# Kernel optimization log

Hardware: AMD Instinct MI355X
Metric: run time of the kernel (lower is better)

## Reference

```python
import jax, jax.numpy as jnp
import numpy as np

M_B, M_S, D_IN, D_OUT = 4, 2048, 4096, 4096
SPARSITY_KEEP = 0.1


def setup_inputs() -> dict:
    key = jax.random.key(0)
    k1, k2, k3, k4 = jax.random.split(key, 4)
    data = jax.random.normal(k1, (M_B, M_S, D_IN), dtype=jnp.float32)
    weight = jax.random.normal(k2, (D_OUT, D_IN), dtype=jnp.float32) * 0.02
    w_mask = (jax.random.uniform(k3, (D_OUT, D_IN)) < SPARSITY_KEEP).astype(jnp.float32)
    bias_p = jax.random.normal(k4, (D_OUT,), dtype=jnp.float32) * 0.02
    return {"data": data, "weight": weight, "w_mask": w_mask, "bias_p": bias_p}


def reference(data, weight, w_mask, bias_p):
    # Equivalent math to CSR-conversion + sparse GEMM: out = data @ (W*mask)^T + b
    w = weight * w_mask                      # [D_OUT, D_IN]
    out = jnp.einsum('bsk,nk->bsn', data, w)  # [B, S, D_OUT]
    return out + bias_p
```

## Files before the change

### kernel.cpp

```cpp
#include <hip/hip_runtime.h>
#include <hip/hip_bf16.h>


#define M_TOT 8192
#define N_TOT 4096
#define K_TOT 4096

#define BM 256
#define BN 256
#define BK 64
#define NT (K_TOT / BK)

typedef __attribute__((ext_vector_type(8))) short short8;
typedef __attribute__((ext_vector_type(4))) float floatx4;

__device__ inline unsigned short f2bf(float f) {
    unsigned int u = __builtin_bit_cast(unsigned int, f);
    u += 0x7fffu + ((u >> 16) & 1u);
    return (unsigned short)(u >> 16);
}

__global__ __launch_bounds__(256) void cast_data_kernel(const float4* __restrict__ in,
                                                        ushort4* __restrict__ out) {
    int i = blockIdx.x * 256 + threadIdx.x;
    float4 f = in[i];
    ushort4 o;
    o.x = f2bf(f.x); o.y = f2bf(f.y); o.z = f2bf(f.z); o.w = f2bf(f.w);
    out[i] = o;
}

__global__ __launch_bounds__(256) void cast_w_kernel(const float4* __restrict__ w,
                                                     const float4* __restrict__ m,
                                                     ushort4* __restrict__ out) {
    int i = blockIdx.x * 256 + threadIdx.x;
    float4 a = w[i];
    float4 b = m[i];
    ushort4 o;
    o.x = f2bf(a.x * b.x); o.y = f2bf(a.y * b.y);
    o.z = f2bf(a.z * b.z); o.w = f2bf(a.w * b.w);
    out[i] = o;
}

__device__ inline void load_lds16(const unsigned short* g, unsigned short* l) {
    __builtin_amdgcn_global_load_lds(
        (__attribute__((address_space(1))) void*)(const_cast<unsigned short*>(g)),
        (__attribute__((address_space(3))) void*)(l),
        16, 0, 0);
}

#define BAR()   __builtin_amdgcn_s_barrier()
#define SB0()   __builtin_amdgcn_sched_barrier(0)
#define VM8()   asm volatile("s_waitcnt vmcnt(8)" ::: "memory")
#define VM0()   asm volatile("s_waitcnt vmcnt(0)" ::: "memory")

__global__ __launch_bounds__(512, 2) void gemm_bt_kernel(const unsigned short* __restrict__ A,
                                                         const unsigned short* __restrict__ W,
                                                         const float* __restrict__ bias,
                                                         float* __restrict__ out) {
    __shared__ __align__(16) unsigned short As[2 * BM * BK];
    __shared__ __align__(16) unsigned short Bs[2 * BN * BK];

    const int t = threadIdx.x;
    const int m0 = blockIdx.y * BM;
    const int n0 = blockIdx.x * BN;

    const int lane  = t & 63;
    const int wv    = t >> 6;
    const int wm    = (wv >> 2) * 128;
    const int wn    = (wv & 3) * 64;
    const int row16 = lane & 15;
    const int quad  = lane >> 4;
    const int rx    = row16 & 7;

    const int srow  = t >> 3;
    const int lslot = (t & 7) ^ (srow & 7);
    const size_t thr_off = (size_t)srow * K_TOT + (size_t)lslot * 8;

    const unsigned short* Ag = A + (size_t)m0 * K_TOT + thr_off;
    const unsigned short* Bg = W + (size_t)n0 * K_TOT + thr_off;

    auto stageA = [&](int ts, int h) {
        const unsigned short* s = Ag + (size_t)(h * 128) * K_TOT + ts * BK;
        unsigned short* d = As + (ts & 1) * (BM * BK) + h * (128 * BK) + t * 8;
        load_lds16(s, d);
        load_lds16(s + (size_t)64 * K_TOT, d + 512 * 8);
    };
    auto stageB = [&](int ts, int h) {
        const unsigned short* s = Bg + (size_t)(h * 128) * K_TOT + ts * BK;
        unsigned short* d = Bs + (ts & 1) * (BN * BK) + h * (128 * BK) + t * 8;
        load_lds16(s, d);
        load_lds16(s + (size_t)64 * K_TOT, d + 512 * 8);
    };

    short8 aX[4][2], aY[4][2];
    short8 b0[2][2], b1[2][2];

    auto readA = [&](int buf, int mh, short8 (&d)[4][2]) {
#pragma unroll
        for (int i = 0; i < 4; i++) {
            const unsigned short* base =
                As + buf * (BM * BK) + (wm + mh * 64 + i * 16 + row16) * BK;
            d[i][0] = *(const short8*)(base + ((quad ^ rx) << 3));
            d[i][1] = *(const short8*)(base + (((4 + quad) ^ rx) << 3));
        }
    };
    auto readB = [&](int buf, int nh, short8 (&d)[2][2]) {
#pragma unroll
        for (int j = 0; j < 2; j++) {
            const unsigned short* base =
                Bs + buf * (BN * BK) + (wn + nh * 32 + j * 16 + row16) * BK;
            d[j][0] = *(const short8*)(base + ((quad ^ rx) << 3));
            d[j][1] = *(const short8*)(base + (((4 + quad) ^ rx) << 3));
        }
    };

    floatx4 acc[8][4];
#pragma unroll
    for (int i = 0; i < 8; i++)
#pragma unroll
        for (int j = 0; j < 4; j++) {
            floatx4 z = {0.0f, 0.0f, 0.0f, 0.0f};
            acc[i][j] = z;
        }

    auto mmaQ = [&](short8 (&a)[4][2], short8 (&b)[2][2], int mh, int nh) {
        __builtin_amdgcn_s_setprio(1);
#pragma unroll
        for (int i = 0; i < 4; i++)
#pragma unroll
            for (int j = 0; j < 2; j++)
#pragma unroll
                for (int ks = 0; ks < 2; ks++)
                    acc[mh * 4 + i][nh * 2 + j] = __builtin_amdgcn_mfma_f32_16x16x32_bf16(
                        a[i][ks], b[j][ks], acc[mh * 4 + i][nh * 2 + j], 0, 0, 0);
        __builtin_amdgcn_s_setprio(0);
    };

    auto tileT = [&](int kt, short8 (&aC)[4][2], short8 (&aN)[4][2], int mode) {
        const int buf = kt & 1;
        readA(buf, 1, aN);
        mmaQ(aC, b0, 0, 0);
        if (mode != 2) BAR();
        readB(buf, 1, b1);
        if (mode == 0) { stageA(kt + 2, 0); stageB(kt + 2, 0); }
        mmaQ(aN, b0, 1, 0);
        if (mode != 2) BAR();
        if (mode == 0) stageA(kt + 2, 1);
        mmaQ(aN, b1, 1, 1);
        if (mode != 2) BAR();
        if (mode == 0) { stageB(kt + 2, 1); VM8(); }
        else if (mode == 1) { VM0(); }
        if (mode != 2) {
            BAR(); SB0();
            readA(buf ^ 1, 0, aN);
            readB(buf ^ 1, 0, b0);
        }
        mmaQ(aC, b1, 0, 1);
        if (mode != 2) BAR();
    };

    stageA(0, 0); stageB(0, 0); stageA(0, 1); stageB(0, 1);
    stageA(1, 0); stageB(1, 0); stageA(1, 1); stageB(1, 1);
    VM8();
    BAR(); SB0();
    readA(0, 0, aX);
    readB(0, 0, b0);

    for (int kt = 0; kt < NT - 2; kt += 2) {
        tileT(kt,     aX, aY, 0);
        tileT(kt + 1, aY, aX, 0);
    }
    tileT(NT - 2, aX, aY, 1);
    tileT(NT - 1, aY, aX, 2);

    float bb[4];
#pragma unroll
    for (int j = 0; j < 4; j++)
        bb[j] = bias[n0 + wn + j * 16 + row16];

#pragma unroll
    for (int ai = 0; ai < 8; ai++) {
        const int gm = m0 + wm + ai * 16 + quad * 4;
#pragma unroll
        for (int bj = 0; bj < 4; bj++) {
            const int gn = n0 + wn + bj * 16 + row16;
            float* o = out + (size_t)gm * N_TOT + gn;
#pragma unroll
            for (int r = 0; r < 4; r++)
                o[(size_t)r * N_TOT] = acc[ai][bj][r] + bb[bj];
        }
    }
}

extern "C" void kernel_launch(void* const* d_in, const int* in_sizes, int n_in,
                              void* d_out, int out_size, void* d_ws, size_t ws_size,
                              hipStream_t stream) {
    const float* data   = (const float*)d_in[0];
    const float* weight = (const float*)d_in[1];
    const float* w_mask = (const float*)d_in[2];
    const float* bias_p = (const float*)d_in[3];
    float* out = (float*)d_out;

    unsigned short* a_bf = (unsigned short*)d_ws;
    unsigned short* w_bf = a_bf + (size_t)M_TOT * K_TOT;

    cast_data_kernel<<<(M_TOT * K_TOT) / (256 * 4), 256, 0, stream>>>(
        (const float4*)data, (ushort4*)a_bf);
    cast_w_kernel<<<(N_TOT * K_TOT) / (256 * 4), 256, 0, stream>>>(
        (const float4*)weight, (const float4*)w_mask, (ushort4*)w_bf);

    dim3 grid(N_TOT / BN, M_TOT / BM);
    gemm_bt_kernel<<<grid, 512, 0, stream>>>(a_bf, w_bf, bias_p, out);
}
```

Before: 529.9 us.

## Switch GEMM to 32x32x16 MFMA tiles and rework prefetch/barrier schedule

Replaces the 16x16x32 bf16 MFMA fragments with 32x32x16 MFMAs, which changes the LDS read pattern, the register fragment layout and the output write mapping. It also reorders the global-to-LDS staging so that A and B are each issued as a group, uses a vmcnt(4) wait, and removes one barrier per tile. The larger MFMA shape is meant to cut LDS read traffic and instruction count per FLOP. The removed barrier and the reordered waits change the synchronization between LDS buffer reuse and the prefetch, which risks races or stalls.

```diff
diff --git a/kernel.cpp b/kernel.cpp
--- a/kernel.cpp
+++ b/kernel.cpp
@@ -12,7 +12,7 @@
 #define NT (K_TOT / BK)
 
 typedef __attribute__((ext_vector_type(8))) short short8;
-typedef __attribute__((ext_vector_type(4))) float floatx4;
+typedef __attribute__((ext_vector_type(16))) float floatx16;
 
 __device__ inline unsigned short f2bf(float f) {
     unsigned int u = __builtin_bit_cast(unsigned int, f);
@@ -51,6 +51,7 @@
 #define BAR()   __builtin_amdgcn_s_barrier()
 #define SB0()   __builtin_amdgcn_sched_barrier(0)
 #define VM8()   asm volatile("s_waitcnt vmcnt(8)" ::: "memory")
+#define VM4()   asm volatile("s_waitcnt vmcnt(4)" ::: "memory")
 #define VM0()   asm volatile("s_waitcnt vmcnt(0)" ::: "memory")
 
 __global__ __launch_bounds__(512, 2) void gemm_bt_kernel(const unsigned short* __restrict__ A,
@@ -68,9 +69,9 @@
     const int wv    = t >> 6;
     const int wm    = (wv >> 2) * 128;
     const int wn    = (wv & 3) * 64;
-    const int row16 = lane & 15;
-    const int quad  = lane >> 4;
-    const int rx    = row16 & 7;
+    const int l31   = lane & 31;
+    const int khalf = lane >> 5;
+    const int rx    = lane & 7;
 
     const int srow  = t >> 3;
     const int lslot = (t & 7) ^ (srow & 7);
@@ -92,66 +93,62 @@
         load_lds16(s + (size_t)64 * K_TOT, d + 512 * 8);
     };
 
-    short8 aX[4][2], aY[4][2];
-    short8 b0[2][2], b1[2][2];
-
-    auto readA = [&](int buf, int mh, short8 (&d)[4][2]) {
-#pragma unroll
-        for (int i = 0; i < 4; i++) {
+    short8 aX[8], aY[8];
+    short8 b0[4], b1[4];
+
+    auto readA = [&](int buf, int mh, short8 (&d)[8]) {
+#pragma unroll
+        for (int mf = 0; mf < 2; mf++) {
             const unsigned short* base =
-                As + buf * (BM * BK) + (wm + mh * 64 + i * 16 + row16) * BK;
-            d[i][0] = *(const short8*)(base + ((quad ^ rx) << 3));
-            d[i][1] = *(const short8*)(base + (((4 + quad) ^ rx) << 3));
-        }
-    };
-    auto readB = [&](int buf, int nh, short8 (&d)[2][2]) {
+                As + buf * (BM * BK) + (wm + mh * 64 + mf * 32 + l31) * BK;
+#pragma unroll
+            for (int ks = 0; ks < 4; ks++)
+                d[mf * 4 + ks] = *(const short8*)(base + (((ks * 2 + khalf) ^ rx) << 3));
+        }
+    };
+    auto readB = [&](int buf, int nh, short8 (&d)[4]) {
+        const unsigned short* base =
+            Bs + buf * (BN * BK) + (wn + nh * 32 + l31) * BK;
+#pragma unroll
+        for (int ks = 0; ks < 4; ks++)
+            d[ks] = *(const short8*)(base + (((ks * 2 + khalf) ^ rx) << 3));
+    };
+
+    floatx16 acc[4][2];
+#pragma unroll
+    for (int i = 0; i < 4; i++)
 #pragma unroll
         for (int j = 0; j < 2; j++) {
-            const unsigned short* base =
-                Bs + buf * (BN * BK) + (wn + nh * 32 + j * 16 + row16) * BK;
-            d[j][0] = *(const short8*)(base + ((quad ^ rx) << 3));
-            d[j][1] = *(const short8*)(base + (((4 + quad) ^ rx) << 3));
-        }
-    };
-
-    floatx4 acc[8][4];
-#pragma unroll
-    for (int i = 0; i < 8; i++)
-#pragma unroll
-        for (int j = 0; j < 4; j++) {
-            floatx4 z = {0.0f, 0.0f, 0.0f, 0.0f};
+            floatx16 z = {0,0,0,0,0,0,0,0,0,0,0,0,0,0,0,0};
             acc[i][j] = z;
         }
 
-    auto mmaQ = [&](short8 (&a)[4][2], short8 (&b)[2][2], int mh, int nh) {
+    auto mmaQ = [&](short8 (&a)[8], short8 (&b)[4], int mh, int nh) {
         __builtin_amdgcn_s_setprio(1);
 #pragma unroll
-        for (int i = 0; i < 4; i++)
-#pragma unroll
-            for (int j = 0; j < 2; j++)
-#pragma unroll
-                for (int ks = 0; ks < 2; ks++)
-                    acc[mh * 4 + i][nh * 2 + j] = __builtin_amdgcn_mfma_f32_16x16x32_bf16(
-                        a[i][ks], b[j][ks], acc[mh * 4 + i][nh * 2 + j], 0, 0, 0);
+        for (int mf = 0; mf < 2; mf++)
+#pragma unroll
+            for (int ks = 0; ks < 4; ks++)
+                acc[mh * 2 + mf][nh] = __builtin_amdgcn_mfma_f32_32x32x16_bf16(
+                    a[mf * 4 + ks], b[ks], acc[mh * 2 + mf][nh], 0, 0, 0);
         __builtin_amdgcn_s_setprio(0);
     };
 
-    auto tileT = [&](int kt, short8 (&aC)[4][2], short8 (&aN)[4][2], int mode) {
+    auto tileT = [&](int kt, short8 (&aC)[8], short8 (&aN)[8], int mode) {
         const int buf = kt & 1;
         readA(buf, 1, aN);
         mmaQ(aC, b0, 0, 0);
         if (mode != 2) BAR();
         readB(buf, 1, b1);
-        if (mode == 0) { stageA(kt + 2, 0); stageB(kt + 2, 0); }
         mmaQ(aN, b0, 1, 0);
         if (mode != 2) BAR();
-        if (mode == 0) stageA(kt + 2, 1);
+        if (mode == 0) { stageA(kt + 2, 0); stageA(kt + 2, 1); VM4(); }
+        else if (mode == 1) { VM0(); }
         mmaQ(aN, b1, 1, 1);
         if (mode != 2) BAR();
-        if (mode == 0) { stageB(kt + 2, 1); VM8(); }
-        else if (mode == 1) { VM0(); }
+        if (mode == 0) { stageB(kt + 2, 0); stageB(kt + 2, 1); }
         if (mode != 2) {
-            BAR(); SB0();
+            SB0();
             readA(buf ^ 1, 0, aN);
             readB(buf ^ 1, 0, b0);
         }
@@ -159,8 +156,8 @@
         if (mode != 2) BAR();
     };
 
-    stageA(0, 0); stageB(0, 0); stageA(0, 1); stageB(0, 1);
-    stageA(1, 0); stageB(1, 0); stageA(1, 1); stageB(1, 1);
+    stageA(0, 0); stageA(0, 1); stageB(0, 0); stageB(0, 1);
+    stageA(1, 0); stageA(1, 1); stageB(1, 0); stageB(1, 1);
     VM8();
     BAR(); SB0();
     readA(0, 0, aX);
@@ -173,21 +170,22 @@
     tileT(NT - 2, aX, aY, 1);
     tileT(NT - 1, aY, aX, 2);
 
-    float bb[4];
-#pragma unroll
-    for (int j = 0; j < 4; j++)
-        bb[j] = bias[n0 + wn + j * 16 + row16];
-
-#pragma unroll
-    for (int ai = 0; ai < 8; ai++) {
-        const int gm = m0 + wm + ai * 16 + quad * 4;
-#pragma unroll
-        for (int bj = 0; bj < 4; bj++) {
-            const int gn = n0 + wn + bj * 16 + row16;
-            float* o = out + (size_t)gm * N_TOT + gn;
-#pragma unroll
-            for (int r = 0; r < 4; r++)
-                o[(size_t)r * N_TOT] = acc[ai][bj][r] + bb[bj];
+    float bb[2];
+#pragma unroll
+    for (int an = 0; an < 2; an++)
+        bb[an] = bias[n0 + wn + an * 32 + l31];
+
+#pragma unroll
+    for (int am = 0; am < 4; am++) {
+        const int gmb = m0 + wm + am * 32 + 4 * khalf;
+#pragma unroll
+        for (int an = 0; an < 2; an++) {
+            const int gn = n0 + wn + an * 32 + l31;
+#pragma unroll
+            for (int reg = 0; reg < 16; reg++) {
+                const int gr = gmb + (reg & 3) + 8 * (reg >> 2);
+                out[(size_t)gr * N_TOT + gn] = acc[am][an][reg] + bb[an];
+            }
         }
     }
 }
```

Measured after the change: 554.8 us. 1.05x slower.
